# Kernel tuning notes

Measured on AMD Instinct MI355X. Metric: run time of the kernel, lower is better.

Reference implementation:

```python
import jax, jax.numpy as jnp
import numpy as np

EMBED_DIM = 1024
NUM_HEADS = 16
HEAD_DIM = 64


def setup_inputs() -> dict:
    key = jax.random.key(0)
    k_x, k_wqkv, k_bqkv, k_wo, k_bo = jax.random.split(key, 5)
    hd = NUM_HEADS * HEAD_DIM
    x = jax.random.normal(k_x, (2, 2048, EMBED_DIM), dtype=jnp.float32)
    # nn.Linear-style init scale
    s1 = 1.0 / np.sqrt(EMBED_DIM)
    s2 = 1.0 / np.sqrt(hd)
    W_qkv = jax.random.uniform(k_wqkv, (EMBED_DIM, 3 * hd), jnp.float32, -s1, s1)
    b_qkv = jax.random.uniform(k_bqkv, (3 * hd,), jnp.float32, -s1, s1)
    W_out = jax.random.uniform(k_wo, (hd, EMBED_DIM), jnp.float32, -s2, s2)
    b_out = jax.random.uniform(k_bo, (EMBED_DIM,), jnp.float32, -s2, s2)
    return {"x": x, "W_qkv": W_qkv, "b_qkv": b_qkv, "W_out": W_out, "b_out": b_out}


def reference(x, W_qkv, b_qkv, W_out, b_out):
    b, s, _ = x.shape
    h, d = NUM_HEADS, HEAD_DIM
    qkv = x @ W_qkv + b_qkv                      # [b, s, 3*h*d]
    qkv = qkv.reshape(b, s, 3, h, d)             # packed order (three, h, d)
    q, k, v = qkv[:, :, 0], qkv[:, :, 1], qkv[:, :, 2]  # each [b, s, h, d]
    scale = 1.0 / jnp.sqrt(jnp.asarray(d, x.dtype))
    scores = jnp.einsum('bshd,bthd->bhst', q, k) * scale  # [b, h, s, s]
    probs = jax.nn.softmax(scores, axis=-1)
    out = jnp.einsum('bhst,bthd->bshd', probs, v)          # [b, s, h, d]
    out = out.reshape(b, s, h * d)
    return out @ W_out + b_out                   # [b, s, embed_dim]
```

## Files before the change

kernel.cpp:

```cpp
#include <hip/hip_runtime.h>

typedef __attribute__((ext_vector_type(8))) short short8;
typedef __attribute__((ext_vector_type(4))) float f32x4;
typedef unsigned short u16;
typedef unsigned int u32;
typedef unsigned long long u64;

#define EMBED 1024
#define SEQ 2048
#define NH 16
#define HD 64

#define MFMA(a, b, c) __builtin_amdgcn_mfma_f32_16x16x32_bf16(a, b, c, 0, 0, 0)

__device__ __forceinline__ u16 f2bf(float f) {
  union { float f; u32 u; } v; v.f = f;
  u32 r = v.u + 0x7fffu + ((v.u >> 16) & 1u);
  return (u16)(r >> 16);
}

__device__ __forceinline__ u32 cvtpk(float lo, float hi) {
  u32 r;
  asm("v_cvt_pk_bf16_f32 %0, %1, %2" : "=v"(r) : "v"(lo), "v"(hi));
  return r;
}

__device__ __forceinline__ float ex2(float x) { return __builtin_amdgcn_exp2f(x); }

__device__ __forceinline__ void async16(const void* g, void* l) {
  __builtin_amdgcn_global_load_lds(
      (const __attribute__((address_space(1))) void*)(uintptr_t)g,
      (__attribute__((address_space(3))) void*)(u32)(uintptr_t)l, 16, 0, 0);
}

__global__ __launch_bounds__(256) void prep_kernel(
    const float* __restrict__ x, u16* __restrict__ xb,
    const float* __restrict__ Wq, u16* __restrict__ Wqt,
    const float* __restrict__ Wo, u16* __restrict__ Wot) {
  int bx = blockIdx.x;
  if (bx < 4096) {
    int i = bx * 256 + threadIdx.x;
    float4 v = ((const float4*)x)[i];
    u64 pk = (u64)f2bf(v.x) | ((u64)f2bf(v.y) << 16) | ((u64)f2bf(v.z) << 32) |
             ((u64)f2bf(v.w) << 48);
    ((u64*)xb)[i] = pk;
    return;
  }
  __shared__ float tile[32][33];
  const int K = 1024;
  int bx2 = bx - 4096;
  int nb = bx2 & 127, kb = bx2 >> 7;
  const float* W; u16* Wt; int N, n0;
  if (nb < 96) { W = Wq; Wt = Wqt; N = 3072; n0 = nb * 32; }
  else         { W = Wo; Wt = Wot; N = 1024; n0 = (nb - 96) * 32; }
  int k0 = kb * 32;
  int tx = threadIdx.x & 31, ty = threadIdx.x >> 5;
#pragma unroll
  for (int p = 0; p < 4; ++p)
    tile[ty + 8 * p][tx] = W[(u64)(k0 + ty + 8 * p) * N + n0 + tx];
  __syncthreads();
#pragma unroll
  for (int p = 0; p < 4; ++p)
    Wt[(u64)(n0 + ty + 8 * p) * K + k0 + tx] = f2bf(tile[tx][ty + 8 * p]);
}

__global__ __launch_bounds__(256) void gemm_qkv_kernel(
    const u16* __restrict__ A, const u16* __restrict__ Bt, const float* __restrict__ bias,
    u16* __restrict__ qb, u16* __restrict__ kb, u16* __restrict__ vtb) {
  __shared__ u16 As[2][128 * 32];
  __shared__ u16 Bs[2][128 * 32];
  const int K = 1024;
  int m0 = blockIdx.y * 128, n0 = blockIdx.x * 128;
  int tid = threadIdx.x, w = tid >> 6, lane = tid & 63;
  int wm = w >> 1, wn = w & 1;
  int c = lane & 15, g = lane >> 4;

  f32x4 acc[4][4] = {};

  int srow = lane >> 2;
  int scol = (lane & 3) * 8;
  const u16* a0 = A + (u64)m0 * K;
  const u16* b0 = Bt + (u64)n0 * K;

  auto stage = [&](int buf, int kt) {
#pragma unroll
    for (int i = 0; i < 2; ++i) {
      int chunk = w * 2 + i;
      int row = chunk * 16 + srow;
      async16(a0 + (u64)row * K + kt + scol, (char*)As[buf] + chunk * 1024 + lane * 16);
      async16(b0 + (u64)row * K + kt + scol, (char*)Bs[buf] + chunk * 1024 + lane * 16);
    }
  };

  auto body = [&](int cur, int kt, bool last) {
    if (!last) {
      stage(cur ^ 1, kt + 32);
      asm volatile("s_waitcnt vmcnt(4)" ::: "memory");
    } else {
      asm volatile("s_waitcnt vmcnt(0)" ::: "memory");
    }
    __builtin_amdgcn_s_barrier();
    asm volatile("" ::: "memory");
    short8 af[4], bfr[4];
#pragma unroll
    for (int i = 0; i < 4; ++i)
      af[i] = *(const short8*)(As[cur] + (wm * 64 + i * 16 + c) * 32 + g * 8);
#pragma unroll
    for (int j = 0; j < 4; ++j)
      bfr[j] = *(const short8*)(Bs[cur] + (wn * 64 + j * 16 + c) * 32 + g * 8);
#pragma unroll
    for (int i = 0; i < 4; ++i)
#pragma unroll
      for (int j = 0; j < 4; ++j)
        acc[i][j] = MFMA(af[i], bfr[j], acc[i][j]);
    asm volatile("s_waitcnt lgkmcnt(0)" ::: "memory");
    __builtin_amdgcn_s_barrier();
    asm volatile("" ::: "memory");
  };

  stage(0, 0);
  for (int kt = 0; kt < K; kt += 64) {
    body(0, kt, false);
    body(1, kt + 32, kt + 64 >= K);
  }

  const float QSCALE = 0.125f * 1.44269504f;
#pragma unroll
  for (int j = 0; j < 4; ++j) {
    int col = n0 + wn * 64 + j * 16 + c;
    float bv = bias[col];
    int sel = col >> 10;
    int h = (col & 1023) >> 6, d = col & 63;
#pragma unroll
    for (int i = 0; i < 4; ++i) {
      int rowb = m0 + wm * 64 + i * 16 + g * 4;
      int b = rowb >> 11, s = rowb & 2047;
      int bh = b * NH + h;
      if (sel == 0) {
#pragma unroll
        for (int r = 0; r < 4; ++r)
          qb[((u64)bh * SEQ + (s + r)) * HD + d] = f2bf((acc[i][j][r] + bv) * QSCALE);
      } else if (sel == 1) {
#pragma unroll
        for (int r = 0; r < 4; ++r)
          kb[((u64)bh * SEQ + (s + r)) * HD + d] = f2bf(acc[i][j][r] + bv);
      } else {
        u64 pk = 0;
#pragma unroll
        for (int r = 0; r < 4; ++r) pk |= (u64)f2bf(acc[i][j][r] + bv) << (16 * r);
        *(u64*)(vtb + ((u64)bh * HD + d) * SEQ + s) = pk;
      }
    }
  }
}

__global__ __launch_bounds__(256, 2) void attn_kernel(const u16* __restrict__ qb,
                                                      const u16* __restrict__ kb,
                                                      const u16* __restrict__ vtb,
                                                      u16* __restrict__ aout) {
  __shared__ __align__(16) u16 Ks[2][64 * 64];
  __shared__ __align__(16) u16 Vts[2][64 * 64];
  __shared__ __align__(16) u16 Pb[4][32 * 64];
  int bid = blockIdx.x;
  int wg = (bid & 7) * 64 + (bid >> 3);
  int bh = wg >> 4;
  int q0 = (wg & 15) * 128;
  int tid = threadIdx.x, w = tid >> 6, lane = tid & 63;
  int c = lane & 15, g = lane >> 4;

  const u16* Qb = qb + ((u64)bh * SEQ + q0 + w * 32) * HD;
  short8 qf[2][2];
#pragma unroll
  for (int i = 0; i < 2; ++i)
#pragma unroll
    for (int ks = 0; ks < 2; ++ks)
      qf[i][ks] = *(const short8*)(Qb + (i * 16 + c) * HD + ks * 32 + g * 8);

  f32x4 o[2][4] = {};
  f32x4 lacc[2] = {};

  int sr = lane >> 3;
  int se = 8 * ((lane & 7) ^ sr);
  char* Pw = (char*)&Pb[w][0] + c * 128;
  u32 pswz = (c & 7) << 4;
  const u16* kbase = kb + (u64)bh * SEQ * HD;
  const u16* vbase = vtb + (u64)bh * HD * SEQ;

  auto stage = [&](int buf, int t0) {
#pragma unroll
    for (int i = 0; i < 2; ++i) {
      int chunk = w * 2 + i;
      int row = chunk * 8 + sr;
      async16(kbase + (u64)(t0 + row) * HD + se,
              (char*)Ks[buf] + chunk * 1024 + lane * 16);
      async16(vbase + (u64)row * SEQ + t0 + se,
              (char*)Vts[buf] + chunk * 1024 + lane * 16);
    }
  };

  auto body = [&](int cur, int t0, bool last) {
    if (!last) {
      stage(cur ^ 1, t0 + 64);
      asm volatile("s_waitcnt vmcnt(4)" ::: "memory");
    } else {
      asm volatile("s_waitcnt vmcnt(0)" ::: "memory");
    }
    __builtin_amdgcn_s_barrier();
    asm volatile("" ::: "memory");

    const u16* KsC = Ks[cur];
    const u16* VtsC = Vts[cur];

    f32x4 s0[4] = {}, s1[4] = {};
    __builtin_amdgcn_s_setprio(1);
#pragma unroll
    for (int j = 0; j < 4; ++j) {
      int trow = j * 16 + c;
      int sw = (trow & 7) << 4;
#pragma unroll
      for (int ks = 0; ks < 2; ++ks) {
        short8 ak = *(const short8*)((const char*)KsC + trow * 128 +
                                     ((g * 16 + ks * 64) ^ sw));
        s0[j] = MFMA(ak, qf[0][ks], s0[j]);
        s1[j] = MFMA(ak, qf[1][ks], s1[j]);
      }
    }
    __builtin_amdgcn_s_setprio(0);

#pragma unroll
    for (int j = 0; j < 4; ++j)
#pragma unroll
      for (int r = 0; r < 4; ++r) {
        s0[j][r] = ex2(s0[j][r]);
        s1[j][r] = ex2(s1[j][r]);
      }
    lacc[0] += (s0[0] + s0[1]) + (s0[2] + s0[3]);
    lacc[1] += (s1[0] + s1[1]) + (s1[2] + s1[3]);

    {
      u64 a0 = (u64)cvtpk(s0[0][0], s0[0][1]) | ((u64)cvtpk(s0[0][2], s0[0][3]) << 32);
      u64 a1 = (u64)cvtpk(s0[1][0], s0[1][1]) | ((u64)cvtpk(s0[1][2], s0[1][3]) << 32);
      u64 a2 = (u64)cvtpk(s0[2][0], s0[2][1]) | ((u64)cvtpk(s0[2][2], s0[2][3]) << 32);
      u64 a3 = (u64)cvtpk(s0[3][0], s0[3][1]) | ((u64)cvtpk(s0[3][2], s0[3][3]) << 32);
      *(u64*)(Pw + ((g * 8 + 0)  ^ pswz)) = a0;
      *(u64*)(Pw + ((g * 8 + 32) ^ pswz)) = a1;
      *(u64*)(Pw + ((g * 8 + 64) ^ pswz)) = a2;
      *(u64*)(Pw + ((g * 8 + 96) ^ pswz)) = a3;
      u64 b0 = (u64)cvtpk(s1[0][0], s1[0][1]) | ((u64)cvtpk(s1[0][2], s1[0][3]) << 32);
      u64 b1 = (u64)cvtpk(s1[1][0], s1[1][1]) | ((u64)cvtpk(s1[1][2], s1[1][3]) << 32);
      u64 b2 = (u64)cvtpk(s1[2][0], s1[2][1]) | ((u64)cvtpk(s1[2][2], s1[2][3]) << 32);
      u64 b3 = (u64)cvtpk(s1[3][0], s1[3][1]) | ((u64)cvtpk(s1[3][2], s1[3][3]) << 32);
      *(u64*)(Pw + 2048 + ((g * 8 + 0)  ^ pswz)) = b0;
      *(u64*)(Pw + 2048 + ((g * 8 + 32) ^ pswz)) = b1;
      *(u64*)(Pw + 2048 + ((g * 8 + 64) ^ pswz)) = b2;
      *(u64*)(Pw + 2048 + ((g * 8 + 96) ^ pswz)) = b3;
    }

    __builtin_amdgcn_s_setprio(1);
#pragma unroll
    for (int ks = 0; ks < 2; ++ks) {
      short8 pa0 = *(const short8*)(Pw + ((ks * 64 + g * 16) ^ pswz));
      short8 pa1 = *(const short8*)(Pw + 2048 + ((ks * 64 + g * 16) ^ pswz));
#pragma unroll
      for (int jd = 0; jd < 4; ++jd) {
        int drow = jd * 16 + c;
        int sw = (drow & 7) << 4;
        short8 bv = *(const short8*)((const char*)VtsC + drow * 128 +
                                     ((g * 16 + ks * 64) ^ sw));
        o[0][jd] = MFMA(pa0, bv, o[0][jd]);
        o[1][jd] = MFMA(pa1, bv, o[1][jd]);
      }
    }
    __builtin_amdgcn_s_setprio(0);

    asm volatile("s_waitcnt lgkmcnt(0)" ::: "memory");
    __builtin_amdgcn_s_barrier();
    asm volatile("" ::: "memory");
  };

  stage(0, 0);
  const int NT = SEQ / 64;
  for (int it = 0; it < NT; it += 2) {
    body(0, it * 64, false);
    body(1, it * 64 + 64, it + 2 >= NT);
  }

  int hh = bh & 15, b = bh >> 4;
#pragma unroll
  for (int i = 0; i < 2; ++i) {
    float l = (lacc[i][0] + lacc[i][1]) + (lacc[i][2] + lacc[i][3]);
    l += __shfl_xor(l, 16);
    l += __shfl_xor(l, 32);
    float inv = 1.0f / l;
    float invr[4];
#pragma unroll
    for (int r = 0; r < 4; ++r) invr[r] = __shfl(inv, g * 4 + r);
#pragma unroll
    for (int r = 0; r < 4; ++r) {
      int q = q0 + w * 32 + i * 16 + g * 4 + r;
#pragma unroll
      for (int jd = 0; jd < 4; ++jd)
        aout[(u64)(b * SEQ + q) * EMBED + hh * HD + jd * 16 + c] =
            f2bf(o[i][jd][r] * invr[r]);
    }
  }
}

__global__ __launch_bounds__(256) void gemm_out_kernel(const u16* __restrict__ A,
                                                       const u16* __restrict__ Bt,
                                                       const float* __restrict__ bias,
                                                       float* __restrict__ out) {
  __shared__ u16 As[2][128 * 32];
  __shared__ u16 Bs[2][64 * 32];
  const int K = 1024;
  int m0 = blockIdx.y * 128, n0 = blockIdx.x * 64;
  int tid = threadIdx.x, w = tid >> 6, lane = tid & 63;
  int wm = w >> 1, wn = w & 1;
  int c = lane & 15, g = lane >> 4;

  f32x4 acc[4][2] = {};
  int srow = lane >> 2;
  int scol = (lane & 3) * 8;
  const u16* a0 = A + (u64)m0 * K;
  const u16* b0 = Bt + (u64)n0 * K;

  auto stage = [&](int buf, int kt) {
#pragma unroll
    for (int i = 0; i < 2; ++i) {
      int chunk = w * 2 + i;
      int row = chunk * 16 + srow;
      async16(a0 + (u64)row * K + kt + scol, (char*)As[buf] + chunk * 1024 + lane * 16);
    }
    int brow = w * 16 + srow;
    async16(b0 + (u64)brow * K + kt + scol, (char*)Bs[buf] + w * 1024 + lane * 16);
  };

  auto body = [&](int cur, int kt, bool last) {
    if (!last) {
      stage(cur ^ 1, kt + 32);
      asm volatile("s_waitcnt vmcnt(3)" ::: "memory");
    } else {
      asm volatile("s_waitcnt vmcnt(0)" ::: "memory");
    }
    __builtin_amdgcn_s_barrier();
    asm volatile("" ::: "memory");
    short8 af[4], bfr[2];
#pragma unroll
    for (int i = 0; i < 4; ++i)
      af[i] = *(const short8*)(As[cur] + (wm * 64 + i * 16 + c) * 32 + g * 8);
#pragma unroll
    for (int j = 0; j < 2; ++j)
      bfr[j] = *(const short8*)(Bs[cur] + (wn * 32 + j * 16 + c) * 32 + g * 8);
#pragma unroll
    for (int i = 0; i < 4; ++i)
#pragma unroll
      for (int j = 0; j < 2; ++j)
        acc[i][j] = MFMA(af[i], bfr[j], acc[i][j]);
    asm volatile("s_waitcnt lgkmcnt(0)" ::: "memory");
    __builtin_amdgcn_s_barrier();
    asm volatile("" ::: "memory");
  };

  stage(0, 0);
  for (int kt = 0; kt < K; kt += 64) {
    body(0, kt, false);
    body(1, kt + 32, kt + 64 >= K);
  }

#pragma unroll
  for (int j = 0; j < 2; ++j) {
    int col = n0 + wn * 32 + j * 16 + c;
    float bv = bias[col];
#pragma unroll
    for (int i = 0; i < 4; ++i) {
      int rowb = m0 + wm * 64 + i * 16 + g * 4;
#pragma unroll
      for (int r = 0; r < 4; ++r)
        out[(u64)(rowb + r) * EMBED + col] = acc[i][j][r] + bv;
    }
  }
}

extern "C" void kernel_launch(void* const* d_in, const int* in_sizes, int n_in,
                              void* d_out, int out_size, void* d_ws, size_t ws_size,
                              hipStream_t stream) {
  const float* x = (const float*)d_in[0];
  const float* Wqkv = (const float*)d_in[1];
  const float* bqkv = (const float*)d_in[2];
  const float* Wout = (const float*)d_in[3];
  const float* bout = (const float*)d_in[4];
  float* out = (float*)d_out;
  char* ws = (char*)d_ws;

  u16* xb  = (u16*)(ws);
  u16* wqt = (u16*)(ws + (8ull << 20));
  u16* wot = (u16*)(ws + (14ull << 20));
  u16* qb  = (u16*)(ws + (16ull << 20));
  u16* kb  = (u16*)(ws + (24ull << 20));
  u16* vtb = (u16*)(ws + (32ull << 20));
  u16* aout = xb;

  prep_kernel<<<dim3(8192), dim3(256), 0, stream>>>(x, xb, Wqkv, wqt, Wout, wot);
  gemm_qkv_kernel<<<dim3(24, 32), dim3(256), 0, stream>>>(xb, wqt, bqkv, qb, kb, vtb);
  attn_kernel<<<dim3(512), dim3(256), 0, stream>>>(qb, kb, vtb, aout);
  gemm_out_kernel<<<dim3(16, 32), dim3(256), 0, stream>>>(aout, wot, bout, out);
}
```

Measured before the change: 116.2 us.

## Triple-buffer GEMM loads and remap blocks for XCD-aware L2 locality

Both GEMM kernels move from double to triple buffering, so two K-tiles are prefetched ahead, with adjusted vmcnt waits and a fully unrolled loop. Launches become 1D grids, and block IDs are remapped so consecutive blocks on the same XCD (bid & 7) share A rows. The aim is to hide global memory latency and improve L2 reuse of A and B tiles. The cost is more LDS per block, which may lower occupancy, plus a larger unrolled code footprint.

Measured after the change: 108.4 us, median of 2. 6.8% less time.

```diff
diff --git a/kernel.cpp b/kernel.cpp
--- a/kernel.cpp
+++ b/kernel.cpp
@@ -67,10 +67,12 @@
 __global__ __launch_bounds__(256) void gemm_qkv_kernel(
     const u16* __restrict__ A, const u16* __restrict__ Bt, const float* __restrict__ bias,
     u16* __restrict__ qb, u16* __restrict__ kb, u16* __restrict__ vtb) {
-  __shared__ u16 As[2][128 * 32];
-  __shared__ u16 Bs[2][128 * 32];
+  __shared__ u16 As[3][128 * 32];
+  __shared__ u16 Bs[3][128 * 32];
   const int K = 1024;
-  int m0 = blockIdx.y * 128, n0 = blockIdx.x * 128;
+  int bid = blockIdx.x;
+  int wg = (bid & 7) * 96 + (bid >> 3);
+  int m0 = (wg / 24) * 128, n0 = (wg % 24) * 128;
   int tid = threadIdx.x, w = tid >> 6, lane = tid & 63;
   int wm = w >> 1, wn = w & 1;
   int c = lane & 15, g = lane >> 4;
@@ -92,9 +94,15 @@
     }
   };
 
-  auto body = [&](int cur, int kt, bool last) {
-    if (!last) {
-      stage(cur ^ 1, kt + 32);
+  stage(0, 0);
+  stage(1, 32);
+#pragma unroll
+  for (int it = 0; it < 32; ++it) {
+    int cur = it % 3;
+    if (it + 2 < 32) {
+      stage((it + 2) % 3, (it + 2) * 32);
+      asm volatile("s_waitcnt vmcnt(8)" ::: "memory");
+    } else if (it + 1 < 32) {
       asm volatile("s_waitcnt vmcnt(4)" ::: "memory");
     } else {
       asm volatile("s_waitcnt vmcnt(0)" ::: "memory");
@@ -116,12 +124,6 @@
     asm volatile("s_waitcnt lgkmcnt(0)" ::: "memory");
     __builtin_amdgcn_s_barrier();
     asm volatile("" ::: "memory");
-  };
-
-  stage(0, 0);
-  for (int kt = 0; kt < K; kt += 64) {
-    body(0, kt, false);
-    body(1, kt + 32, kt + 64 >= K);
   }
 
   const float QSCALE = 0.125f * 1.44269504f;
@@ -310,10 +312,12 @@
                                                        const u16* __restrict__ Bt,
                                                        const float* __restrict__ bias,
                                                        float* __restrict__ out) {
-  __shared__ u16 As[2][128 * 32];
-  __shared__ u16 Bs[2][64 * 32];
+  __shared__ u16 As[3][128 * 32];
+  __shared__ u16 Bs[3][64 * 32];
   const int K = 1024;
-  int m0 = blockIdx.y * 128, n0 = blockIdx.x * 64;
+  int bid = blockIdx.x;
+  int wg = (bid & 7) * 64 + (bid >> 3);
+  int m0 = (wg >> 4) * 128, n0 = (wg & 15) * 64;
   int tid = threadIdx.x, w = tid >> 6, lane = tid & 63;
   int wm = w >> 1, wn = w & 1;
   int c = lane & 15, g = lane >> 4;
@@ -335,9 +339,15 @@
     async16(b0 + (u64)brow * K + kt + scol, (char*)Bs[buf] + w * 1024 + lane * 16);
   };
 
-  auto body = [&](int cur, int kt, bool last) {
-    if (!last) {
-      stage(cur ^ 1, kt + 32);
+  stage(0, 0);
+  stage(1, 32);
+#pragma unroll
+  for (int it = 0; it < 32; ++it) {
+    int cur = it % 3;
+    if (it + 2 < 32) {
+      stage((it + 2) % 3, (it + 2) * 32);
+      asm volatile("s_waitcnt vmcnt(6)" ::: "memory");
+    } else if (it + 1 < 32) {
       asm volatile("s_waitcnt vmcnt(3)" ::: "memory");
     } else {
       asm volatile("s_waitcnt vmcnt(0)" ::: "memory");
@@ -359,12 +369,6 @@
     asm volatile("s_waitcnt lgkmcnt(0)" ::: "memory");
     __builtin_amdgcn_s_barrier();
     asm volatile("" ::: "memory");
-  };
-
-  stage(0, 0);
-  for (int kt = 0; kt < K; kt += 64) {
-    body(0, kt, false);
-    body(1, kt + 32, kt + 64 >= K);
   }
 
 #pragma unroll
@@ -401,7 +405,7 @@
   u16* aout = xb;
 
   prep_kernel<<<dim3(8192), dim3(256), 0, stream>>>(x, xb, Wqkv, wqt, Wout, wot);
-  gemm_qkv_kernel<<<dim3(24, 32), dim3(256), 0, stream>>>(xb, wqt, bqkv, qb, kb, vtb);
+  gemm_qkv_kernel<<<dim3(768), dim3(256), 0, stream>>>(xb, wqt, bqkv, qb, kb, vtb);
   attn_kernel<<<dim3(512), dim3(256), 0, stream>>>(qb, kb, vtb, aout);
-  gemm_out_kernel<<<dim3(16, 32), dim3(256), 0, stream>>>(aout, wot, bout, out);
-}
+  gemm_out_kernel<<<dim3(512), dim3(256), 0, stream>>>(aout, wot, bout, out);
+}
```
